# Kernel optimization log

Hardware: AMD Instinct MI355X
Metric: run time of the kernel (lower is better)

Reference implementation:

```python
import jax, jax.numpy as jnp
import numpy as np

B, T, P, D, H = 32, 64, 196, 768, 12
HD = D // H   # MHA head dim = 64
F = D // H    # GAT per-head out features = 64


def _grid_adj(num_patches):
    g = int(np.sqrt(num_patches))
    a = np.zeros((num_patches, num_patches), np.int32)
    for i in range(num_patches):
        a[i, i] = 1
        r, c = divmod(i, g)
        for dr in (-1, 0, 1):
            for dc in (-1, 0, 1):
                if dr == 0 and dc == 0:
                    continue
                nr, nc = r + dr, c + dc
                if 0 <= nr < g and 0 <= nc < g:
                    a[i, nr * g + nc] = 1
    return a


def setup_inputs():
    key = jax.random.key(0)
    ks = jax.random.split(key, 32)
    s = 0.02
    ta = jax.random.randint(ks[2], (B, T, T), 0, 2).astype(jnp.int32)
    ta = jnp.maximum(jnp.maximum(ta, ta.transpose(0, 2, 1)), jnp.eye(T, dtype=jnp.int32))
    return {
        'text_features': jax.random.normal(ks[0], (B, T, D), jnp.float32),
        'image_features': jax.random.normal(ks[1], (B, P, D), jnp.float32),
        'clip_text': jax.random.normal(ks[3], (B, 512), jnp.float32),
        'clip_image': jax.random.normal(ks[4], (B, 512), jnp.float32),
        'logit_scale': jnp.float32(4.6052),  # ln(100), CLIP default
        'wq': jax.random.normal(ks[5], (D, D), jnp.float32) * s,
        'bq': jnp.zeros((D,), jnp.float32),
        'wk': jax.random.normal(ks[6], (D, D), jnp.float32) * s,
        'bk': jnp.zeros((D,), jnp.float32),
        'wv': jax.random.normal(ks[7], (D, D), jnp.float32) * s,
        'bv': jnp.zeros((D,), jnp.float32),
        'wo': jax.random.normal(ks[8], (D, D), jnp.float32) * s,
        'bo': jnp.zeros((D,), jnp.float32),
        'Wt': jax.random.normal(ks[9], (D, H * F), jnp.float32) * s,
        'at': jax.random.normal(ks[10], (2 * F, 1), jnp.float32) * s,
        'Wi': jax.random.normal(ks[11], (D, H * F), jnp.float32) * s,
        'ai': jax.random.normal(ks[12], (2 * F, 1), jnp.float32) * s,
        'Wp': jax.random.normal(ks[13], (512, D), jnp.float32) * s,
        'bp': jnp.zeros((D,), jnp.float32),
        'f1w': jax.random.normal(ks[14], (3, 16), jnp.float32) * 0.3,
        'f1b': jnp.zeros((16,), jnp.float32),
        'f2w': jax.random.normal(ks[15], (16, 3), jnp.float32) * 0.3,
        'f2b': jnp.zeros((3,), jnp.float32),
        'c1w': jax.random.normal(ks[16], (D, D // 2), jnp.float32) * s,
        'c1b': jnp.zeros((D // 2,), jnp.float32),
        'c2w': jax.random.normal(ks[17], (D // 2, 2), jnp.float32) * s,
        'c2b': jnp.zeros((2,), jnp.float32),
        'text_adj': ta,
        'image_adj': jnp.asarray(_grid_adj(P)),
    }


def _gat(h, adj, W, a):
    # h: [N, D], adj: [N, N] (0/1), W: [D, H*F], a: [2F, 1]
    N = h.shape[0]
    Wh = (h @ W).reshape(N, H, F)
    # e_ij = leakyrelu(a^T [Wh_i ; Wh_j]) decomposed to avoid the N*N*2F concat tensor
    src = jnp.einsum('nhf,f->nh', Wh, a[:F, 0])   # [N, H]
    dst = jnp.einsum('nhf,f->nh', Wh, a[F:, 0])   # [N, H]
    e = jax.nn.leaky_relu(src[:, None, :] + dst[None, :, :], 0.2)  # [N, N, H]
    e = jnp.where(adj[:, :, None] > 0, e, jnp.float32(-9e15))
    att = jax.nn.softmax(e, axis=1)               # softmax over neighbors j
    hp = jnp.einsum('ijh,jhf->ihf', att, Wh)       # [N, H, F]
    return jax.nn.elu(hp.reshape(N, H * F))


def reference(text_features, image_features, clip_text, clip_image, logit_scale,
              wq, bq, wk, bk, wv, bv, wo, bo, Wt, at, Wi, ai, Wp, bp,
              f1w, f1b, f2w, f2b, c1w, c1b, c2w, c2b, text_adj, image_adj):
    # token-level cross attention (text queries, image keys/values)
    q = (text_features @ wq + bq).reshape(B, T, H, HD)
    k = (image_features @ wk + bk).reshape(B, P, H, HD)
    v = (image_features @ wv + bv).reshape(B, P, H, HD)
    scores = jnp.einsum('bthd,bphd->bhtp', q, k) / jnp.sqrt(jnp.float32(HD))
    upd = jnp.einsum('bhtp,bphd->bthd', jax.nn.softmax(scores, axis=-1), v)
    upd = upd.reshape(B, T, D) @ wo + bo           # [B, T, D]
    c = jnp.einsum('btd,bpd->btp', upd, image_features)
    s_token = jnp.mean(jnp.diagonal(c, axis1=-2, axis2=-1), axis=1)  # [B]
    f_token = upd.mean(axis=1)                     # [B, D]
    # per-sample GATs, batched via vmap
    tg = jax.vmap(lambda h, a_: _gat(h, a_, Wt, at))(text_features, text_adj)
    ig = jax.vmap(lambda h: _gat(h, image_adj, Wi, ai))(image_features)
    tgf = tg.mean(axis=1)
    igf = ig.mean(axis=1)

    def cos(x, y):
        nx = jnp.maximum(jnp.linalg.norm(x, axis=-1), 1e-8)
        ny = jnp.maximum(jnp.linalg.norm(y, axis=-1), 1e-8)
        return jnp.sum(x * y, axis=-1) / (nx * ny)

    s_phrase = cos(tgf, igf)
    s_global = jnp.exp(logit_scale) * cos(clip_text, clip_image)
    f_global = clip_text @ Wp + bp
    scores3 = jax.lax.stop_gradient(jnp.stack([s_token, s_phrase, s_global], axis=1))
    w = jax.nn.sigmoid(jax.nn.gelu(scores3 @ f1w + f1b, approximate=False) @ f2w + f2b)
    f_agg = w[:, 0:1] * f_token + w[:, 1:2] * tgf + w[:, 2:3] * f_global
    logits = jax.nn.relu(f_agg @ c1w + c1b) @ c2w + c2b  # dropout inactive (eval)
    return logits
```

## Files before the change

### kernel.cpp

```cpp
#include <hip/hip_runtime.h>
#include <hip/hip_bf16.h>
#include <math.h>

#define B 32
#define T 64
#define P 196
#define D 768
#define H 12

typedef __attribute__((ext_vector_type(8))) short short8;
typedef __attribute__((ext_vector_type(4))) float floatx4;

__device__ __forceinline__ float wave_sum(float v) {
#pragma unroll
  for (int o = 32; o > 0; o >>= 1) v += __shfl_xor(v, o);
  return v;
}
__device__ __forceinline__ unsigned short f2bf(float x) {
  unsigned u = __float_as_uint(x);
  u += 0x7FFFu + ((u >> 16) & 1u);
  return (unsigned short)(u >> 16);
}
__device__ __forceinline__ float bf2f(unsigned short x) {
  return __uint_as_float((unsigned)x << 16);
}
__device__ __forceinline__ float fexp(float x) { return __expf(x); }
__device__ __forceinline__ float frcp(float x) { return __builtin_amdgcn_rcpf(x); }
__device__ __forceinline__ void async_cp16(const unsigned short* g, unsigned short* l) {
  __builtin_amdgcn_global_load_lds(
      (const __attribute__((address_space(1))) unsigned int*)g,
      (__attribute__((address_space(3))) unsigned int*)l, 16, 0, 0);
}
__device__ __forceinline__ int xcd_remap(int orig, int nwg) {
  const int q = nwg >> 3, r = nwg & 7;
  const int x = orig & 7, o = orig >> 3;
  return (x < r ? x * (q + 1) : r * (q + 1) + (x - r) * q) + o;
}

struct WPack {
  const float* src[6];
  unsigned short* dst[6];
};
__global__ __launch_bounds__(256) void prep_kernel(
    WPack p,
    const float* __restrict__ text, unsigned short* __restrict__ text_bf, int n40,
    const float* __restrict__ img, unsigned short* __restrict__ img_bf, int n41,
    const float* __restrict__ bq, const float* __restrict__ bk,
    const float* __restrict__ bv,
    float* __restrict__ bt, float* __restrict__ bi, float* __restrict__ stok) {
  const int bid = blockIdx.x;
  if (bid < 3456) {
    __shared__ float tile[32][33];
    const int z = bid / 576, rem = bid % 576;
    const int bx = rem % 24, by = rem / 24;
    const float* W = p.src[z];
    unsigned short* Wt = p.dst[z];
    const int tx = threadIdx.x & 31, ty = threadIdx.x >> 5;
    const int n0 = bx * 32, k0 = by * 32;
#pragma unroll
    for (int r = 0; r < 4; ++r)
      tile[ty + 8 * r][tx] = W[(size_t)(k0 + ty + 8 * r) * D + n0 + tx];
    __syncthreads();
#pragma unroll
    for (int r = 0; r < 4; ++r)
      Wt[(size_t)(n0 + ty + 8 * r) * D + k0 + tx] = f2bf(tile[tx][ty + 8 * r]);
  } else if (bid < 9696) {
    int i = (bid - 3456) * 256 + threadIdx.x;
    const float* X;
    unsigned short* Y;
    int idx;
    if (i < n40) { X = text; Y = text_bf; idx = i; }
    else if (i < n40 + n41) { X = img; Y = img_bf; idx = i - n40; }
    else return;
    float4 vv = ((const float4*)X)[idx];
    ushort4 o;
    o.x = f2bf(vv.x); o.y = f2bf(vv.y); o.z = f2bf(vv.z); o.w = f2bf(vv.w);
    ((ushort4*)Y)[idx] = o;
  } else {
    int i = (bid - 9696) * 256 + threadIdx.x;
    if (i < 32) stok[i] = 0.f;
    if (i < 768) { bt[i] = bq[i]; bi[i] = bk[i]; }
    else if (i < 1536) { bt[i] = 0.f; bi[i] = bv[i - 768]; }
    else if (i < 2304) { bi[i] = 0.f; }
  }
}

struct GemmJob {
  const unsigned short* A;
  const unsigned short* Bt;
  const float* bias;
  void* C;
  int N, K, lda, ldb, colTiles;
};

template <bool BF16OUT>
__device__ __forceinline__ void gemm_body(const GemmJob& j, int bx, int by, int tid) {
  __shared__ unsigned short As[3][128][32];
  __shared__ unsigned short Bs[3][128][32];
  const int lane = tid & 63;
  const int w = tid >> 6;
  const int quad = lane >> 4;
  const int l15 = lane & 15;
  const int row0 = by * 128;
  const int col0 = bx * 128;
  const int m_off = (w & 1) * 64;
  const int n_off = (w >> 1) * 64;
  const int N = j.N, K = j.K;

  const int srow = 16 * w + (lane >> 2);
  const int scol = (((lane & 3) ^ ((lane >> 3) & 3))) * 8;
  const unsigned short* gA0 = j.A + (size_t)(row0 + srow) * j.lda + scol;
  const unsigned short* gA1 = j.A + (size_t)(row0 + srow + 64) * j.lda + scol;
  const unsigned short* gB0 = j.Bt + (size_t)(col0 + srow) * j.ldb + scol;
  const unsigned short* gB1 = j.Bt + (size_t)(col0 + srow + 64) * j.ldb + scol;

  const int rdc = (quad ^ ((l15 >> 1) & 3)) * 8;

  floatx4 acc[4][4] = {};
  short8 fA[4], fB_[4];
  short8 gA_[4], gB_[4];

#define STAGE(buf, kk)                                   \
  do {                                                   \
    async_cp16(gA0 + (kk), &As[buf][16 * w][0]);         \
    async_cp16(gA1 + (kk), &As[buf][64 + 16 * w][0]);    \
    async_cp16(gB0 + (kk), &Bs[buf][16 * w][0]);         \
    async_cp16(gB1 + (kk), &Bs[buf][64 + 16 * w][0]);    \
  } while (0)

  auto RD = [&](short8 (&AF)[4], short8 (&BF)[4], int buf) {
#pragma unroll
    for (int i = 0; i < 4; ++i)
      AF[i] = *(const short8*)&As[buf][m_off + 16 * i + l15][rdc];
#pragma unroll
    for (int j2 = 0; j2 < 4; ++j2)
      BF[j2] = *(const short8*)&Bs[buf][n_off + 16 * j2 + l15][rdc];
  };
  auto MM = [&](short8 (&AF)[4], short8 (&BF)[4]) {
#pragma unroll
    for (int i = 0; i < 4; ++i)
#pragma unroll
      for (int j2 = 0; j2 < 4; ++j2)
        acc[i][j2] = __builtin_amdgcn_mfma_f32_16x16x32_bf16(AF[i], BF[j2], acc[i][j2], 0, 0, 0);
  };
  auto PHASE = [&](short8 (&curA)[4], short8 (&curB)[4],
                   short8 (&nxtA)[4], short8 (&nxtB)[4],
                   int stageBuf, int readBuf, int kk) {
    if (kk + 64 < K) {
      STAGE(stageBuf, kk + 64);
      asm volatile("s_waitcnt vmcnt(4) lgkmcnt(0)" ::: "memory");
      __builtin_amdgcn_s_barrier();
      __builtin_amdgcn_sched_barrier(0);
      RD(nxtA, nxtB, readBuf);
    } else if (kk + 32 < K) {
      asm volatile("s_waitcnt vmcnt(0) lgkmcnt(0)" ::: "memory");
      __builtin_amdgcn_s_barrier();
      __builtin_amdgcn_sched_barrier(0);
      RD(nxtA, nxtB, readBuf);
    }
    MM(curA, curB);
  };

  STAGE(0, 0);
  STAGE(1, 32);
  asm volatile("s_waitcnt vmcnt(4)" ::: "memory");
  __builtin_amdgcn_s_barrier();
  __builtin_amdgcn_sched_barrier(0);
  RD(fA, fB_, 0);

  for (int k0 = 0; k0 < K; k0 += 192) {
    PHASE(fA, fB_, gA_, gB_, 2, 1, k0);
    PHASE(gA_, gB_, fA, fB_, 0, 2, k0 + 32);
    PHASE(fA, fB_, gA_, gB_, 1, 0, k0 + 64);
    PHASE(gA_, gB_, fA, fB_, 2, 1, k0 + 96);
    PHASE(fA, fB_, gA_, gB_, 0, 2, k0 + 128);
    PHASE(gA_, gB_, fA, fB_, 1, 0, k0 + 160);
  }
#undef STAGE

#pragma unroll
  for (int jj = 0; jj < 4; ++jj) {
    const int cg = col0 + n_off + 16 * jj + l15;
    const float bv = j.bias ? j.bias[cg] : 0.0f;
#pragma unroll
    for (int i = 0; i < 4; ++i) {
      const int rbase = row0 + m_off + 16 * i + quad * 4;
#pragma unroll
      for (int r = 0; r < 4; ++r) {
        const float val = acc[i][jj][r] + bv;
        const size_t idx = (size_t)(rbase + r) * N + cg;
        if (BF16OUT) ((unsigned short*)j.C)[idx] = f2bf(val);
        else ((float*)j.C)[idx] = val;
      }
    }
  }
}

__global__ __launch_bounds__(256) void gemm_mfma_dual_bf16(GemmJob j0, GemmJob j1,
                                                           int split, int total) {
  const bool first = ((int)blockIdx.x < split);
  const GemmJob& j = first ? j0 : j1;
  const int orig = first ? blockIdx.x : (blockIdx.x - split);
  const int bid = xcd_remap(orig, first ? split : total - split);
  const int bx = bid % j.colTiles;
  const int by = bid / j.colTiles;
  gemm_body<true>(j, bx, by, threadIdx.x);
}

__global__ __launch_bounds__(256) void gemm_mfma_dual_f32(GemmJob j0, GemmJob j1,
                                                          int split, int total) {
  const bool first = ((int)blockIdx.x < split);
  const GemmJob& j = first ? j0 : j1;
  const int orig = first ? blockIdx.x : (blockIdx.x - split);
  const int bid = xcd_remap(orig, first ? split : total - split);
  const int bx = bid % j.colTiles;
  const int by = bid / j.colTiles;
  gemm_body<false>(j, bx, by, threadIdx.x);
}


__device__ __forceinline__ void attn_body(
    char* smem, int h, int b,
    const unsigned short* __restrict__ qa, const unsigned short* __restrict__ kvw,
    unsigned short* __restrict__ attout) {
  const int tid = threadIdx.x, lane = tid & 63, w = tid >> 6;
  const int quad = lane >> 4, l15 = lane & 15;

  unsigned short (*Ks)[72] = (unsigned short(*)[72])smem;
  unsigned short (*Ps)[16][232] = (unsigned short(*)[16][232])smem;
  unsigned short (*VT)[232] = (unsigned short(*)[232])(smem + 29952);

  for (int i = tid; i < P * 8; i += 256) {
    const int p = i >> 3, dg = i & 7;
    const short8 k8 =
        *(const short8*)(kvw + (size_t)(b * P + p) * 2304 + h * 64 + dg * 8);
    *(short8*)&Ks[p][dg * 8] = k8;
  }
  {
    const int d = lane;
    const unsigned short* vbase = kvw + (size_t)b * P * 2304 + 768 + h * 64 + d;
    for (int pb = w; pb < 28; pb += 4) {
      short8 v;
#pragma unroll
      for (int z = 0; z < 8; ++z) {
        const int p = pb * 8 + z;
        v[z] = (p < P) ? (short)vbase[(size_t)p * 2304] : (short)0;
      }
      *(short8*)&VT[d][pb * 8] = v;
    }
  }
  __syncthreads();

  short8 aq[2];
#pragma unroll
  for (int ks = 0; ks < 2; ++ks)
    aq[ks] = *(const short8*)(qa + (size_t)(b * T + 16 * w + l15) * 1536 + h * 64 +
                              32 * ks + quad * 8);

  floatx4 sc[13];
#pragma unroll
  for (int tile = 0; tile < 13; ++tile) {
    int p = tile * 16 + l15;
    if (p > 195) p = 195;
    short8 bk0 = *(const short8*)&Ks[p][quad * 8];
    short8 bk1 = *(const short8*)&Ks[p][32 + quad * 8];
    floatx4 c = {};
    c = __builtin_amdgcn_mfma_f32_16x16x32_bf16(aq[0], bk0, c, 0, 0, 0);
    c = __builtin_amdgcn_mfma_f32_16x16x32_bf16(aq[1], bk1, c, 0, 0, 0);
    sc[tile] = c;
  }

  float mx[4] = {-3.4e38f, -3.4e38f, -3.4e38f, -3.4e38f};
#pragma unroll
  for (int tile = 0; tile < 13; ++tile)
#pragma unroll
    for (int r = 0; r < 4; ++r) {
      float s = sc[tile][r] * 0.125f;
      if (tile == 12 && l15 >= 4) s = -3.0e38f;
      sc[tile][r] = s;
      mx[r] = fmaxf(mx[r], s);
    }
#pragma unroll
  for (int off = 1; off < 16; off <<= 1)
#pragma unroll
    for (int r = 0; r < 4; ++r) mx[r] = fmaxf(mx[r], __shfl_xor(mx[r], off));

  float sm[4] = {};
#pragma unroll
  for (int tile = 0; tile < 13; ++tile)
#pragma unroll
    for (int r = 0; r < 4; ++r) {
      float e = fexp(sc[tile][r] - mx[r]);
      sc[tile][r] = e;
      sm[r] += e;
    }
#pragma unroll
  for (int off = 1; off < 16; off <<= 1)
#pragma unroll
    for (int r = 0; r < 4; ++r) sm[r] += __shfl_xor(sm[r], off);
  float inv[4];
#pragma unroll
  for (int r = 0; r < 4; ++r) inv[r] = frcp(sm[r]);

  __syncthreads();

#pragma unroll
  for (int tile = 0; tile < 13; ++tile)
#pragma unroll
    for (int r = 0; r < 4; ++r)
      Ps[w][quad * 4 + r][tile * 16 + l15] = f2bf(sc[tile][r]);
#pragma unroll
  for (int r = 0; r < 4; ++r)
    Ps[w][quad * 4 + r][208 + l15] = 0;

  floatx4 oc[4] = {};
#pragma unroll
  for (int ks = 0; ks < 7; ++ks) {
    short8 pa = *(const short8*)&Ps[w][l15][ks * 32 + quad * 8];
#pragma unroll
    for (int nt = 0; nt < 4; ++nt) {
      short8 bv = *(const short8*)&VT[nt * 16 + l15][ks * 32 + quad * 8];
      oc[nt] = __builtin_amdgcn_mfma_f32_16x16x32_bf16(pa, bv, oc[nt], 0, 0, 0);
    }
  }

#pragma unroll
  for (int nt = 0; nt < 4; ++nt)
#pragma unroll
    for (int r = 0; r < 4; ++r)
      attout[(size_t)(b * T + 16 * w + quad * 4 + r) * 768 + h * 64 + nt * 16 + l15] =
          f2bf(oc[nt][r] * inv[r]);
}

__device__ __forceinline__ void text_gat_body(
    char* smem, int h, int b,
    const unsigned short* __restrict__ Wh, int ldw, const int* __restrict__ adj,
    const float* __restrict__ at, float* __restrict__ tgf) {
  const int tid = threadIdx.x, lane = tid & 63, w = tid >> 6;
  const int quad = lane >> 4, l15 = lane & 15;

  unsigned short (*VT)[72] = (unsigned short(*)[72])smem;
  unsigned short (*Ps)[16][72] = (unsigned short(*)[16][72])(smem + 9216);
  float* srcs = (float*)(smem + 18432);
  float* dsts = (float*)(smem + 18688);
  float (*redc)[64] = (float(*)[64])(smem + 18944);
  float* asv = (float*)(smem + 19968);
  float* adv = (float*)(smem + 20224);

  if (tid < 64) { asv[tid] = at[tid]; adv[tid] = at[64 + tid]; }
  {
    const int f = lane;
    const unsigned short* wbase = Wh + (size_t)(b * T) * ldw + h * 64 + f;
    for (int nb = w; nb < 8; nb += 4) {
      short8 v;
#pragma unroll
      for (int z = 0; z < 8; ++z)
        v[z] = (short)wbase[(size_t)(nb * 8 + z) * ldw];
      *(short8*)&VT[f][nb * 8] = v;
    }
  }
  __syncthreads();

  if (tid < 64) {
    float s = 0.f, dd = 0.f;
#pragma unroll 8
    for (int f = 0; f < 64; ++f) {
      const float wv = bf2f(VT[f][tid]);
      s += wv * asv[f];
      dd += wv * adv[f];
    }
    srcs[tid] = s;
    dsts[tid] = dd;
  }
  __syncthreads();

  const int i = 16 * w + l15;
  const float si = srcs[i];
  const int* ar = adj + (size_t)b * T * T + i * 64;
  float sm = 0.f;
#pragma unroll 8
  for (int jj = 0; jj < 16; ++jj) {
    const int j = 4 * jj + quad;
    float e = si + dsts[j];
    e = (e >= 0.f) ? e : 0.2f * e;
    const float p = (ar[j] != 0) ? fexp(e) : 0.f;
    sm += p;
    Ps[w][l15][j] = f2bf(p);
  }
  sm += __shfl_xor(sm, 16);
  sm += __shfl_xor(sm, 32);
  const float inv = frcp(sm);

  floatx4 oc[4] = {};
#pragma unroll
  for (int ks = 0; ks < 2; ++ks) {
    const short8 pa = *(const short8*)&Ps[w][l15][ks * 32 + quad * 8];
#pragma unroll
    for (int nt = 0; nt < 4; ++nt) {
      const short8 bv = *(const short8*)&VT[nt * 16 + l15][ks * 32 + quad * 8];
      oc[nt] = __builtin_amdgcn_mfma_f32_16x16x32_bf16(pa, bv, oc[nt], 0, 0, 0);
    }
  }

  float accd[4] = {};
#pragma unroll
  for (int r = 0; r < 4; ++r) {
    const float invr = __shfl(inv, quad * 4 + r);
#pragma unroll
    for (int nt = 0; nt < 4; ++nt) {
      const float hp = oc[nt][r] * invr;
      accd[nt] += (hp > 0.f) ? hp : (fexp(hp) - 1.0f);
    }
  }
#pragma unroll
  for (int nt = 0; nt < 4; ++nt) {
    accd[nt] += __shfl_xor(accd[nt], 16);
    accd[nt] += __shfl_xor(accd[nt], 32);
  }
  if (quad == 0) {
#pragma unroll
    for (int nt = 0; nt < 4; ++nt) redc[w][nt * 16 + l15] = accd[nt];
  }
  __syncthreads();
  if (w == 0) {
    const float tot = redc[0][lane] + redc[1][lane] + redc[2][lane] + redc[3][lane];
    tgf[b * D + h * 64 + lane] = tot * (1.0f / T);
  }
}

__device__ __forceinline__ void image_gat_body(
    char* smem, int h, int b,
    const unsigned short* __restrict__ Wh, int ldw, const float* __restrict__ ai,
    const int* __restrict__ adj, float* __restrict__ igf) {
  const int tid = threadIdx.x, lane = tid & 63, w = tid >> 6;
  const int quad = lane >> 4, l15 = lane & 15;

  unsigned short (*VT)[232] = (unsigned short(*)[232])smem;
  unsigned short (*Ps)[232] = (unsigned short(*)[232])(smem + 29696);
  float* srcs = (float*)(smem + 37120);
  float* dsts = (float*)(smem + 37904);
  float* asv = (float*)(smem + 38688);
  float* adv = (float*)(smem + 38944);

  if (tid < 64) { asv[tid] = ai[tid]; adv[tid] = ai[64 + tid]; }
  {
    const int f = lane;
    const unsigned short* wbase = Wh + (size_t)(b * P) * ldw + h * 64 + f;
    for (int nb = w; nb < 28; nb += 4) {
      short8 v;
#pragma unroll
      for (int z = 0; z < 8; ++z) {
        const int p = nb * 8 + z;
        v[z] = (p < P) ? (short)wbase[(size_t)p * ldw] : (short)0;
      }
      *(short8*)&VT[f][nb * 8] = v;
    }
  }
  __syncthreads();

  if (tid < P) {
    float s = 0.f, dd = 0.f;
#pragma unroll 8
    for (int f = 0; f < 64; ++f) {
      const float wv = bf2f(VT[f][tid]);
      s += wv * asv[f];
      dd += wv * adv[f];
    }
    srcs[tid] = s;
    dsts[tid] = dd;
  }
  __syncthreads();

  const int rloc = tid >> 4;
  const int cslot = tid & 15;
  float accw = 0.f;

  for (int tile = 0; tile < 13; ++tile) {
    const int i = tile * 16 + rloc;
    const int ii = (i < P) ? i : (P - 1);
    const float si = srcs[ii];
    const int* ar = adj + ii * P;
    int msk[13];
#pragma unroll
    for (int k = 0; k < 13; ++k) {
      const int jc = k * 16 + cslot;
      msk[k] = (jc < P) ? ar[jc] : 0;
    }
    float pvv[13];
    float sm = 0.f;
#pragma unroll
    for (int k = 0; k < 13; ++k) {
      const int jc = k * 16 + cslot;
      float p = 0.f;
      if (jc < P && msk[k] != 0) {
        float e = si + dsts[jc];
        e = (e >= 0.f) ? e : 0.2f * e;
        p = fexp(e);
      }
      pvv[k] = p;
      sm += p;
    }
    sm += __shfl_xor(sm, 1);
    sm += __shfl_xor(sm, 2);
    sm += __shfl_xor(sm, 4);
    sm += __shfl_xor(sm, 8);
    const float inv = frcp(sm);
#pragma unroll
    for (int k = 0; k < 13; ++k)
      Ps[rloc][k * 16 + cslot] = f2bf(pvv[k] * inv);
    Ps[rloc][208 + cslot] = 0;
    __syncthreads();

    floatx4 oc = {};
#pragma unroll
    for (int ks = 0; ks < 7; ++ks) {
      const short8 pa = *(const short8*)&Ps[l15][ks * 32 + quad * 8];
      const short8 bvv = *(const short8*)&VT[w * 16 + l15][ks * 32 + quad * 8];
      oc = __builtin_amdgcn_mfma_f32_16x16x32_bf16(pa, bvv, oc, 0, 0, 0);
    }
#pragma unroll
    for (int r = 0; r < 4; ++r) {
      const int io = tile * 16 + quad * 4 + r;
      if (io < P) {
        const float hp = oc[r];
        accw += (hp > 0.f) ? hp : (fexp(hp) - 1.0f);
      }
    }
    __syncthreads();
  }

  accw += __shfl_xor(accw, 16);
  accw += __shfl_xor(accw, 32);
  if (quad == 0)
    igf[b * D + h * 64 + w * 16 + l15] = accw * (1.0f / P);
}

__device__ __forceinline__ void fglob_body(
    char* smem, int jt, int b,
    const float* __restrict__ clip_t, const float* __restrict__ Wp,
    const float* __restrict__ bp, float* __restrict__ fglob) {
  const int j = threadIdx.x & 63, kc = threadIdx.x >> 6;
  float s = 0.f;
  const float* ct = clip_t + b * 512;
#pragma unroll 4
  for (int k = kc * 128; k < kc * 128 + 128; ++k)
    s += ct[k] * Wp[(size_t)k * D + jt * 64 + j];
  float (*red)[64] = (float(*)[64])smem;
  red[kc][j] = s;
  __syncthreads();
  if (kc == 0)
    fglob[b * D + jt * 64 + j] = red[0][j] + red[1][j] + red[2][j] + red[3][j] + bp[jt * 64 + j];
}

__global__ __launch_bounds__(256) void mid_kernel(
    const unsigned short* __restrict__ qa_bf, const unsigned short* __restrict__ kvw_bf,
    unsigned short* __restrict__ att_bf,
    const int* __restrict__ text_adj, const float* __restrict__ at,
    float* __restrict__ tgf,
    const unsigned short* __restrict__ whi, int ldw_i,
    const float* __restrict__ ai, const int* __restrict__ image_adj,
    float* __restrict__ igf,
    const float* __restrict__ clip_t, const float* __restrict__ Wp,
    const float* __restrict__ bp, float* __restrict__ fglob) {
  __shared__ __align__(16) char smem[59648];
  const int h = blockIdx.x, b = blockIdx.y, op = blockIdx.z;
  if (op == 0)
    attn_body(smem, h, b, qa_bf, kvw_bf, att_bf);
  else if (op == 1)
    text_gat_body(smem, h, b, qa_bf + 768, 1536, text_adj, at, tgf);
  else if (op == 2)
    image_gat_body(smem, h, b, whi, ldw_i, ai, image_adj, igf);
  else
    fglob_body(smem, h, b, clip_t, Wp, bp, fglob);
}

__global__ __launch_bounds__(256) void token_kernel(
    const float* __restrict__ upd0, const float* __restrict__ upd1,
    const float* __restrict__ img,
    float* __restrict__ f_token, float* __restrict__ s_token) {
  const int jt = blockIdx.x, b = blockIdx.y;
  const int l = threadIdx.x & 63, tg = threadIdx.x >> 6;
  const int d = jt * 64 + l;
  float fs = 0.f, ss = 0.f;
#pragma unroll 4
  for (int tt = 0; tt < 16; ++tt) {
    const int t = tg * 16 + tt;
    const size_t idx = (size_t)(b * T + t) * D + d;
    const float u = upd0[idx] + upd1[idx];
    fs += u;
    ss += u * img[(size_t)(b * P + t) * D + d];
  }
  __shared__ float red[4][64];
  __shared__ float sred[4];
  red[tg][l] = fs;
  const float sw = wave_sum(ss);
  if (l == 0) sred[tg] = sw;
  __syncthreads();
  if (tg == 0) {
    f_token[(size_t)b * D + d] =
        (red[0][l] + red[1][l] + red[2][l] + red[3][l]) * (1.0f / T);
    if (threadIdx.x == 0)
      atomicAdd(&s_token[b], (sred[0] + sred[1] + sred[2] + sred[3]) * (1.0f / T));
  }
}

__global__ __launch_bounds__(256) void xc1_kernel(
    const float* __restrict__ ftok, const float* __restrict__ tgf,
    const float* __restrict__ fglob, const float* __restrict__ c1w,
    float* __restrict__ Xc) {
  const int jt = blockIdx.x;
  const int r = blockIdx.y;
  const int b = r & 31, which = r >> 5;
  const float* src = (which == 0 ? ftok : which == 1 ? tgf : fglob) + (size_t)b * D;
  const int j = threadIdx.x & 63, kc = threadIdx.x >> 6;
  const int col = jt * 64 + j;
  float s = 0.f;
#pragma unroll 4
  for (int k = kc * 192; k < kc * 192 + 192; ++k)
    s += src[k] * c1w[(size_t)k * 384 + col];
  __shared__ float red[4][64];
  red[kc][j] = s;
  __syncthreads();
  if (kc == 0)
    Xc[(size_t)r * 384 + col] = red[0][j] + red[1][j] + red[2][j] + red[3][j];
}

__device__ __forceinline__ float block_sum(float v, float* red4) {
  v = wave_sum(v);
  __syncthreads();
  if ((threadIdx.x & 63) == 0) red4[threadIdx.x >> 6] = v;
  __syncthreads();
  return red4[0] + red4[1] + red4[2] + red4[3];
}

__global__ __launch_bounds__(256) void final_kernel(
    const float* __restrict__ tgf, const float* __restrict__ igf,
    const float* __restrict__ clip_t, const float* __restrict__ clip_i,
    const float* __restrict__ logit_scale, const float* __restrict__ s_token,
    const float* __restrict__ Xc,
    const float* __restrict__ f1w, const float* __restrict__ f1b,
    const float* __restrict__ f2w, const float* __restrict__ f2b,
    const float* __restrict__ c1b,
    const float* __restrict__ c2w, const float* __restrict__ c2b,
    float* __restrict__ out) {
  const int b = blockIdx.x, tid = threadIdx.x;
  __shared__ float red[4];
  __shared__ float sres[4];
  __shared__ float hid[384];

  float d0 = 0.f, d1 = 0.f, d2 = 0.f;
  for (int i = tid; i < D; i += 256) {
    float x = tgf[b * D + i], y = igf[b * D + i];
    d0 += x * y; d1 += x * x; d2 += y * y;
  }
  float dot_ti = block_sum(d0, red);
  float n_t = sqrtf(block_sum(d1, red));
  float n_i = sqrtf(block_sum(d2, red));
  float s_phrase = dot_ti / (fmaxf(n_t, 1e-8f) * fmaxf(n_i, 1e-8f));

  float c0 = 0.f, c1 = 0.f, c2 = 0.f;
  for (int i = tid; i < 512; i += 256) {
    float x = clip_t[b * 512 + i], y = clip_i[b * 512 + i];
    c0 += x * y; c1 += x * x; c2 += y * y;
  }
  float dc = block_sum(c0, red);
  float nt2 = sqrtf(block_sum(c1, red));
  float ni2 = sqrtf(block_sum(c2, red));
  float s_global = expf(logit_scale[0]) * dc / (fmaxf(nt2, 1e-8f) * fmaxf(ni2, 1e-8f));

  if (tid == 0) {
    float s3[3] = { s_token[b], s_phrase, s_global };
    float h1[16];
    for (int j = 0; j < 16; ++j) {
      float a = f1b[j];
      for (int i2 = 0; i2 < 3; ++i2) a += s3[i2] * f1w[i2 * 16 + j];
      h1[j] = 0.5f * a * (1.0f + erff(a * 0.70710678118654752f));
    }
    for (int j = 0; j < 3; ++j) {
      float a = f2b[j];
      for (int i2 = 0; i2 < 16; ++i2) a += h1[i2] * f2w[i2 * 3 + j];
      sres[j] = 1.0f / (1.0f + expf(-a));
    }
  }
  __syncthreads();
  const float w0 = sres[0], w1 = sres[1], w2 = sres[2];

  for (int j = tid; j < 384; j += 256) {
    const float a = w0 * Xc[(size_t)b * 384 + j] +
                    w1 * Xc[(size_t)(32 + b) * 384 + j] +
                    w2 * Xc[(size_t)(64 + b) * 384 + j] + c1b[j];
    hid[j] = fmaxf(a, 0.0f);
  }
  __syncthreads();

  float p0 = 0.f, p1 = 0.f;
  for (int k2 = tid; k2 < 384; k2 += 256) {
    p0 += hid[k2] * c2w[k2 * 2 + 0];
    p1 += hid[k2] * c2w[k2 * 2 + 1];
  }
  p0 = block_sum(p0, red);
  p1 = block_sum(p1, red);
  if (tid == 0) {
    out[b * 2 + 0] = p0 + c2b[0];
    out[b * 2 + 1] = p1 + c2b[1];
  }
}

extern "C" void kernel_launch(void* const* d_in, const int* in_sizes, int n_in,
                              void* d_out, int out_size, void* d_ws, size_t ws_size,
                              hipStream_t stream) {
  const float* text   = (const float*)d_in[0];
  const float* img    = (const float*)d_in[1];
  const float* clip_t = (const float*)d_in[2];
  const float* clip_i = (const float*)d_in[3];
  const float* lscale = (const float*)d_in[4];
  const float* wq = (const float*)d_in[5];
  const float* bq = (const float*)d_in[6];
  const float* wk = (const float*)d_in[7];
  const float* bk = (const float*)d_in[8];
  const float* wv = (const float*)d_in[9];
  const float* bv = (const float*)d_in[10];
  const float* wo = (const float*)d_in[11];
  const float* bo = (const float*)d_in[12];
  const float* Wt = (const float*)d_in[13];
  const float* at = (const float*)d_in[14];
  const float* Wi = (const float*)d_in[15];
  const float* ai = (const float*)d_in[16];
  const float* Wp = (const float*)d_in[17];
  const float* bp = (const float*)d_in[18];
  const float* f1w = (const float*)d_in[19];
  const float* f1b = (const float*)d_in[20];
  const float* f2w = (const float*)d_in[21];
  const float* f2b = (const float*)d_in[22];
  const float* c1w = (const float*)d_in[23];
  const float* c1b = (const float*)d_in[24];
  const float* c2w = (const float*)d_in[25];
  const float* c2b = (const float*)d_in[26];
  const int* text_adj  = (const int*)d_in[27];
  const int* image_adj = (const int*)d_in[28];
  float* out = (float*)d_out;

  const size_t nTD = (size_t)B * T * D;
  const size_t nPD = (size_t)B * P * D;
  const size_t nWW = (size_t)D * D;

  float* fbuf = (float*)d_ws;
  size_t o = 0;
  float* upd0    = fbuf + o; o += nTD;
  float* upd1    = fbuf + o; o += nTD;
  float* ftok    = fbuf + o; o += (size_t)B * D;
  float* stok    = fbuf + o; o += 32;
  float* tgf     = fbuf + o; o += (size_t)B * D;
  float* igf     = fbuf + o; o += (size_t)B * D;
  float* fglob   = fbuf + o; o += (size_t)B * D;
  float* bcat_t  = fbuf + o; o += 1536;
  float* bcat_i3 = fbuf + o; o += 2304;
  float* Xc      = fbuf + o; o += (size_t)96 * 384;
  unsigned short* sbuf = (unsigned short*)(fbuf + o);
  size_t so = 0;
  unsigned short* kvw_bf    = sbuf + so; so += 3 * nPD;
  unsigned short* qa_bf     = sbuf + so; so += 2 * nTD;
  unsigned short* text_bf   = sbuf + so; so += nTD;
  unsigned short* img_bf    = sbuf + so; so += nPD;
  unsigned short* att_bf    = sbuf + so; so += nTD;
  unsigned short* wcat_txt  = sbuf + so; so += 2 * nWW;
  unsigned short* wcat_img3 = sbuf + so; so += 3 * nWW;
  unsigned short* wo_t      = sbuf + so; so += nWW;

  WPack wp;
  wp.src[0] = wq; wp.dst[0] = wcat_txt;
  wp.src[1] = Wt; wp.dst[1] = wcat_txt + nWW;
  wp.src[2] = wk; wp.dst[2] = wcat_img3;
  wp.src[3] = wv; wp.dst[3] = wcat_img3 + nWW;
  wp.src[4] = Wi; wp.dst[4] = wcat_img3 + 2 * nWW;
  wp.src[5] = wo; wp.dst[5] = wo_t;
  {
    const int n40 = (int)(nTD / 4), n41 = (int)(nPD / 4);
    prep_kernel<<<9708, 256, 0, stream>>>(wp, text, text_bf, n40, img, img_bf, n41,
                                          bq, bk, bv, bcat_t, bcat_i3, stok);
  }

  const int MT = B * T;
  const int MP = B * P;

  GemmJob jimg;
  jimg.A = img_bf; jimg.Bt = wcat_img3; jimg.bias = bcat_i3; jimg.C = kvw_bf;
  jimg.N = 2304; jimg.K = D; jimg.lda = D; jimg.ldb = D; jimg.colTiles = 2304 / 128;
  GemmJob jtxt;
  jtxt.A = text_bf; jtxt.Bt = wcat_txt; jtxt.bias = bcat_t; jtxt.C = qa_bf;
  jtxt.N = 1536; jtxt.K = D; jtxt.lda = D; jtxt.ldb = D; jtxt.colTiles = 1536 / 128;
  const int splitBlocks = (2304 / 128) * (MP / 128);
  const int totalBlocks = splitBlocks + (1536 / 128) * (MT / 128);
  gemm_mfma_dual_bf16<<<totalBlocks, 256, 0, stream>>>(jimg, jtxt, splitBlocks, totalBlocks);

  const unsigned short* whi_bf = kvw_bf + 1536;
  mid_kernel<<<dim3(H, B, 4), 256, 0, stream>>>(
      qa_bf, kvw_bf, att_bf,
      text_adj, at, tgf,
      whi_bf, 2304, ai, image_adj, igf,
      clip_t, Wp, bp, fglob);

  GemmJob jwo0;
  jwo0.A = att_bf; jwo0.Bt = wo_t; jwo0.bias = bo; jwo0.C = upd0;
  jwo0.N = D; jwo0.K = 384; jwo0.lda = D; jwo0.ldb = D; jwo0.colTiles = D / 128;
  GemmJob jwo1;
  jwo1.A = att_bf + 384; jwo1.Bt = wo_t + 384; jwo1.bias = nullptr; jwo1.C = upd1;
  jwo1.N = D; jwo1.K = 384; jwo1.lda = D; jwo1.ldb = D; jwo1.colTiles = D / 128;
  const int woHalf = (D / 128) * (MT / 128);
  gemm_mfma_dual_f32<<<2 * woHalf, 256, 0, stream>>>(jwo0, jwo1, woHalf, 2 * woHalf);

  token_kernel<<<dim3(12, B), 256, 0, stream>>>(upd0, upd1, img, ftok, stok);
  xc1_kernel<<<dim3(6, 96), 256, 0, stream>>>(ftok, tgf, fglob, c1w, Xc);
  final_kernel<<<B, 256, 0, stream>>>(tgf, igf, clip_t, clip_i, lscale, stok, Xc,
                                      f1w, f1b, f2w, f2b, c1b, c2w, c2b, out);
}
```

Measured before the change: 260.9 us.

## Split wo GEMM four-way along K, move fglob to prep kernel

The output-projection GEMM is now split into four K=192 slices instead of two K=384 slices, so more blocks are in flight on the small M=2048 problem, and the token kernel sums four partial buffers. The clip-text projection (fglob) moves out of mid_kernel into extra blocks of prep_kernel, taking it off the attention/GAT stage. The Q-fragment load in attention is hoisted ahead of the K/V shared-memory staging, and the xc1 and fglob dot loops use four independent accumulators. In exchange, two extra fp32 partial buffers must be written and then read back, which adds memory traffic.

```diff
diff --git a/kernel.cpp b/kernel.cpp
--- a/kernel.cpp
+++ b/kernel.cpp
@@ -47,7 +47,9 @@
     const float* __restrict__ img, unsigned short* __restrict__ img_bf, int n41,
     const float* __restrict__ bq, const float* __restrict__ bk,
     const float* __restrict__ bv,
-    float* __restrict__ bt, float* __restrict__ bi, float* __restrict__ stok) {
+    float* __restrict__ bt, float* __restrict__ bi, float* __restrict__ stok,
+    const float* __restrict__ clip_t, const float* __restrict__ Wp,
+    const float* __restrict__ bp, float* __restrict__ fglob) {
   const int bid = blockIdx.x;
   if (bid < 3456) {
     __shared__ float tile[32][33];
@@ -76,12 +78,32 @@
     ushort4 o;
     o.x = f2bf(vv.x); o.y = f2bf(vv.y); o.z = f2bf(vv.z); o.w = f2bf(vv.w);
     ((ushort4*)Y)[idx] = o;
-  } else {
+  } else if (bid < 9708) {
     int i = (bid - 9696) * 256 + threadIdx.x;
     if (i < 32) stok[i] = 0.f;
     if (i < 768) { bt[i] = bq[i]; bi[i] = bk[i]; }
     else if (i < 1536) { bt[i] = 0.f; bi[i] = bv[i - 768]; }
     else if (i < 2304) { bi[i] = 0.f; }
+  } else {
+    __shared__ float red[4][64];
+    const int bid2 = bid - 9708;
+    const int jt = bid2 % 12, b = bid2 / 12;
+    const int j = threadIdx.x & 63, kc = threadIdx.x >> 6;
+    const float* ct = clip_t + b * 512 + kc * 128;
+    const float* wp = Wp + (size_t)(kc * 128) * D + jt * 64 + j;
+    float s0 = 0.f, s1 = 0.f, s2 = 0.f, s3 = 0.f;
+#pragma unroll
+    for (int k = 0; k < 128; k += 4) {
+      s0 += ct[k]     * wp[(size_t)k * D];
+      s1 += ct[k + 1] * wp[(size_t)(k + 1) * D];
+      s2 += ct[k + 2] * wp[(size_t)(k + 2) * D];
+      s3 += ct[k + 3] * wp[(size_t)(k + 3) * D];
+    }
+    red[kc][j] = (s0 + s1) + (s2 + s3);
+    __syncthreads();
+    if (kc == 0)
+      fglob[b * D + jt * 64 + j] =
+          red[0][j] + red[1][j] + red[2][j] + red[3][j] + bp[jt * 64 + j];
   }
 }
 
@@ -207,12 +229,13 @@
   gemm_body<true>(j, bx, by, threadIdx.x);
 }
 
-__global__ __launch_bounds__(256) void gemm_mfma_dual_f32(GemmJob j0, GemmJob j1,
-                                                          int split, int total) {
-  const bool first = ((int)blockIdx.x < split);
-  const GemmJob& j = first ? j0 : j1;
-  const int orig = first ? blockIdx.x : (blockIdx.x - split);
-  const int bid = xcd_remap(orig, first ? split : total - split);
+__global__ __launch_bounds__(256) void gemm_mfma_quad_f32(GemmJob j0, GemmJob j1,
+                                                          GemmJob j2, GemmJob j3,
+                                                          int per) {
+  const int which = (int)blockIdx.x / per;
+  const GemmJob& j = (which == 0) ? j0 : (which == 1) ? j1 : (which == 2) ? j2 : j3;
+  const int orig = (int)blockIdx.x - which * per;
+  const int bid = xcd_remap(orig, per);
   const int bx = bid % j.colTiles;
   const int by = bid / j.colTiles;
   gemm_body<false>(j, bx, by, threadIdx.x);
@@ -230,6 +253,12 @@
   unsigned short (*Ps)[16][232] = (unsigned short(*)[16][232])smem;
   unsigned short (*VT)[232] = (unsigned short(*)[232])(smem + 29952);
 
+  short8 aq[2];
+#pragma unroll
+  for (int ks = 0; ks < 2; ++ks)
+    aq[ks] = *(const short8*)(qa + (size_t)(b * T + 16 * w + l15) * 1536 + h * 64 +
+                              32 * ks + quad * 8);
+
   for (int i = tid; i < P * 8; i += 256) {
     const int p = i >> 3, dg = i & 7;
     const short8 k8 =
@@ -250,12 +279,6 @@
     }
   }
   __syncthreads();
-
-  short8 aq[2];
-#pragma unroll
-  for (int ks = 0; ks < 2; ++ks)
-    aq[ks] = *(const short8*)(qa + (size_t)(b * T + 16 * w + l15) * 1536 + h * 64 +
-                              32 * ks + quad * 8);
 
   floatx4 sc[13];
 #pragma unroll
@@ -535,23 +558,6 @@
     igf[b * D + h * 64 + w * 16 + l15] = accw * (1.0f / P);
 }
 
-__device__ __forceinline__ void fglob_body(
-    char* smem, int jt, int b,
-    const float* __restrict__ clip_t, const float* __restrict__ Wp,
-    const float* __restrict__ bp, float* __restrict__ fglob) {
-  const int j = threadIdx.x & 63, kc = threadIdx.x >> 6;
-  float s = 0.f;
-  const float* ct = clip_t + b * 512;
-#pragma unroll 4
-  for (int k = kc * 128; k < kc * 128 + 128; ++k)
-    s += ct[k] * Wp[(size_t)k * D + jt * 64 + j];
-  float (*red)[64] = (float(*)[64])smem;
-  red[kc][j] = s;
-  __syncthreads();
-  if (kc == 0)
-    fglob[b * D + jt * 64 + j] = red[0][j] + red[1][j] + red[2][j] + red[3][j] + bp[jt * 64 + j];
-}
-
 __global__ __launch_bounds__(256) void mid_kernel(
     const unsigned short* __restrict__ qa_bf, const unsigned short* __restrict__ kvw_bf,
     unsigned short* __restrict__ att_bf,
@@ -559,23 +565,20 @@
     float* __restrict__ tgf,
     const unsigned short* __restrict__ whi, int ldw_i,
     const float* __restrict__ ai, const int* __restrict__ image_adj,
-    float* __restrict__ igf,
-    const float* __restrict__ clip_t, const float* __restrict__ Wp,
-    const float* __restrict__ bp, float* __restrict__ fglob) {
+    float* __restrict__ igf) {
   __shared__ __align__(16) char smem[59648];
   const int h = blockIdx.x, b = blockIdx.y, op = blockIdx.z;
   if (op == 0)
     attn_body(smem, h, b, qa_bf, kvw_bf, att_bf);
   else if (op == 1)
     text_gat_body(smem, h, b, qa_bf + 768, 1536, text_adj, at, tgf);
-  else if (op == 2)
+  else
     image_gat_body(smem, h, b, whi, ldw_i, ai, image_adj, igf);
-  else
-    fglob_body(smem, h, b, clip_t, Wp, bp, fglob);
 }
 
 __global__ __launch_bounds__(256) void token_kernel(
     const float* __restrict__ upd0, const float* __restrict__ upd1,
+    const float* __restrict__ upd2, const float* __restrict__ upd3,
     const float* __restrict__ img,
     float* __restrict__ f_token, float* __restrict__ s_token) {
   const int jt = blockIdx.x, b = blockIdx.y;
@@ -586,7 +589,7 @@
   for (int tt = 0; tt < 16; ++tt) {
     const int t = tg * 16 + tt;
     const size_t idx = (size_t)(b * T + t) * D + d;
-    const float u = upd0[idx] + upd1[idx];
+    const float u = (upd0[idx] + upd1[idx]) + (upd2[idx] + upd3[idx]);
     fs += u;
     ss += u * img[(size_t)(b * P + t) * D + d];
   }
@@ -614,12 +617,18 @@
   const float* src = (which == 0 ? ftok : which == 1 ? tgf : fglob) + (size_t)b * D;
   const int j = threadIdx.x & 63, kc = threadIdx.x >> 6;
   const int col = jt * 64 + j;
-  float s = 0.f;
-#pragma unroll 4
-  for (int k = kc * 192; k < kc * 192 + 192; ++k)
-    s += src[k] * c1w[(size_t)k * 384 + col];
+  const float* cw = c1w + (size_t)(kc * 192) * 384 + col;
+  const float* sk = src + kc * 192;
+  float s0 = 0.f, s1 = 0.f, s2 = 0.f, s3 = 0.f;
+#pragma unroll 12
+  for (int k = 0; k < 192; k += 4) {
+    s0 += sk[k]     * cw[(size_t)k * 384];
+    s1 += sk[k + 1] * cw[(size_t)(k + 1) * 384];
+    s2 += sk[k + 2] * cw[(size_t)(k + 2) * 384];
+    s3 += sk[k + 3] * cw[(size_t)(k + 3) * 384];
+  }
   __shared__ float red[4][64];
-  red[kc][j] = s;
+  red[kc][j] = (s0 + s1) + (s2 + s3);
   __syncthreads();
   if (kc == 0)
     Xc[(size_t)r * 384 + col] = red[0][j] + red[1][j] + red[2][j] + red[3][j];
@@ -748,6 +757,8 @@
   size_t o = 0;
   float* upd0    = fbuf + o; o += nTD;
   float* upd1    = fbuf + o; o += nTD;
+  float* upd2    = fbuf + o; o += nTD;
+  float* upd3    = fbuf + o; o += nTD;
   float* ftok    = fbuf + o; o += (size_t)B * D;
   float* stok    = fbuf + o; o += 32;
   float* tgf     = fbuf + o; o += (size_t)B * D;
@@ -776,8 +787,9 @@
   wp.src[5] = wo; wp.dst[5] = wo_t;
   {
     const int n40 = (int)(nTD / 4), n41 = (int)(nPD / 4);
-    prep_kernel<<<9708, 256, 0, stream>>>(wp, text, text_bf, n40, img, img_bf, n41,
-                                          bq, bk, bv, bcat_t, bcat_i3, stok);
+    prep_kernel<<<10092, 256, 0, stream>>>(wp, text, text_bf, n40, img, img_bf, n41,
+                                           bq, bk, bv, bcat_t, bcat_i3, stok,
+                                           clip_t, Wp, bp, fglob);
   }
 
   const int MT = B * T;
@@ -794,22 +806,23 @@
   gemm_mfma_dual_bf16<<<totalBlocks, 256, 0, stream>>>(jimg, jtxt, splitBlocks, totalBlocks);
 
   const unsigned short* whi_bf = kvw_bf + 1536;
-  mid_kernel<<<dim3(H, B, 4), 256, 0, stream>>>(
+  mid_kernel<<<dim3(H, B, 3), 256, 0, stream>>>(
       qa_bf, kvw_bf, att_bf,
       text_adj, at, tgf,
-      whi_bf, 2304, ai, image_adj, igf,
-      clip_t, Wp, bp, fglob);
-
-  GemmJob jwo0;
-  jwo0.A = att_bf; jwo0.Bt = wo_t; jwo0.bias = bo; jwo0.C = upd0;
-  jwo0.N = D; jwo0.K = 384; jwo0.lda = D; jwo0.ldb = D; jwo0.colTiles = D / 128;
-  GemmJob jwo1;
-  jwo1.A = att_bf + 384; jwo1.Bt = wo_t + 384; jwo1.bias = nullptr; jwo1.C = upd1;
-  jwo1.N = D; jwo1.K = 384; jwo1.lda = D; jwo1.ldb = D; jwo1.colTiles = D / 128;
-  const int woHalf = (D / 128) * (MT / 128);
-  gemm_mfma_dual_f32<<<2 * woHalf, 256, 0, stream>>>(jwo0, jwo1, woHalf, 2 * woHalf);
-
-  token_kernel<<<dim3(12, B), 256, 0, stream>>>(upd0, upd1, img, ftok, stok);
+      whi_bf, 2304, ai, image_adj, igf);
+
+  GemmJob jw[4];
+  for (int k = 0; k < 4; ++k) {
+    jw[k].A = att_bf + k * 192;
+    jw[k].Bt = wo_t + k * 192;
+    jw[k].bias = (k == 0) ? bo : nullptr;
+    jw[k].C = (k == 0) ? upd0 : (k == 1) ? upd1 : (k == 2) ? upd2 : upd3;
+    jw[k].N = D; jw[k].K = 192; jw[k].lda = D; jw[k].ldb = D; jw[k].colTiles = D / 128;
+  }
+  const int woPer = (D / 128) * (MT / 128);
+  gemm_mfma_quad_f32<<<4 * woPer, 256, 0, stream>>>(jw[0], jw[1], jw[2], jw[3], woPer);
+
+  token_kernel<<<dim3(12, B), 256, 0, stream>>>(upd0, upd1, upd2, upd3, img, ftok, stok);
   xc1_kernel<<<dim3(6, 96), 256, 0, stream>>>(ftok, tgf, fglob, c1w, Xc);
   final_kernel<<<B, 256, 0, stream>>>(tgf, igf, clip_t, clip_i, lscale, stok, Xc,
                                       f1w, f1b, f2w, f2b, c1b, c2w, c2b, out);
```

Result: slower. 270.1 us (+3.5%).

## Split attention out of mid kernel and co-schedule Wo GEMM with GAT branches

Applied to the files above, without the earlier changes.

Attention now runs in its own kernel. The output-projection GEMM is merged into one launch with the text GAT, image GAT and CLIP projection blocks, so the independent GAT work overlaps with the Wo GEMM instead of waiting behind the attention stage. The Q fragment load in attention is also hoisted ahead of the K/V shared-memory staging so its global latency can overlap. The combined kernel sizes shared memory at 48KB for every branch, which assumes the GAT bodies fit in that space, and heterogeneous block types share one launch.

```diff
diff --git a/kernel.cpp b/kernel.cpp
--- a/kernel.cpp
+++ b/kernel.cpp
@@ -94,9 +94,10 @@
 };
 
 template <bool BF16OUT>
-__device__ __forceinline__ void gemm_body(const GemmJob& j, int bx, int by, int tid) {
-  __shared__ unsigned short As[3][128][32];
-  __shared__ unsigned short Bs[3][128][32];
+__device__ __forceinline__ void gemm_body(const GemmJob& j, int bx, int by, int tid,
+                                          char* smem) {
+  unsigned short (*As)[128][32] = (unsigned short(*)[128][32])smem;
+  unsigned short (*Bs)[128][32] = (unsigned short(*)[128][32])(smem + 24576);
   const int lane = tid & 63;
   const int w = tid >> 6;
   const int quad = lane >> 4;
@@ -198,24 +199,14 @@
 
 __global__ __launch_bounds__(256) void gemm_mfma_dual_bf16(GemmJob j0, GemmJob j1,
                                                            int split, int total) {
+  __shared__ __align__(16) char gsmem[49152];
   const bool first = ((int)blockIdx.x < split);
   const GemmJob& j = first ? j0 : j1;
   const int orig = first ? blockIdx.x : (blockIdx.x - split);
   const int bid = xcd_remap(orig, first ? split : total - split);
   const int bx = bid % j.colTiles;
   const int by = bid / j.colTiles;
-  gemm_body<true>(j, bx, by, threadIdx.x);
-}
-
-__global__ __launch_bounds__(256) void gemm_mfma_dual_f32(GemmJob j0, GemmJob j1,
-                                                          int split, int total) {
-  const bool first = ((int)blockIdx.x < split);
-  const GemmJob& j = first ? j0 : j1;
-  const int orig = first ? blockIdx.x : (blockIdx.x - split);
-  const int bid = xcd_remap(orig, first ? split : total - split);
-  const int bx = bid % j.colTiles;
-  const int by = bid / j.colTiles;
-  gemm_body<false>(j, bx, by, threadIdx.x);
+  gemm_body<true>(j, bx, by, threadIdx.x, gsmem);
 }
 
 
@@ -230,6 +221,12 @@
   unsigned short (*Ps)[16][232] = (unsigned short(*)[16][232])smem;
   unsigned short (*VT)[232] = (unsigned short(*)[232])(smem + 29952);
 
+  short8 aq[2];
+#pragma unroll
+  for (int ks = 0; ks < 2; ++ks)
+    aq[ks] = *(const short8*)(qa + (size_t)(b * T + 16 * w + l15) * 1536 + h * 64 +
+                              32 * ks + quad * 8);
+
   for (int i = tid; i < P * 8; i += 256) {
     const int p = i >> 3, dg = i & 7;
     const short8 k8 =
@@ -250,12 +247,6 @@
     }
   }
   __syncthreads();
-
-  short8 aq[2];
-#pragma unroll
-  for (int ks = 0; ks < 2; ++ks)
-    aq[ks] = *(const short8*)(qa + (size_t)(b * T + 16 * w + l15) * 1536 + h * 64 +
-                              32 * ks + quad * 8);
 
   floatx4 sc[13];
 #pragma unroll
@@ -330,6 +321,13 @@
     for (int r = 0; r < 4; ++r)
       attout[(size_t)(b * T + 16 * w + quad * 4 + r) * 768 + h * 64 + nt * 16 + l15] =
           f2bf(oc[nt][r] * inv[r]);
+}
+
+__global__ __launch_bounds__(256) void attn_kernel(
+    const unsigned short* __restrict__ qa_bf, const unsigned short* __restrict__ kvw_bf,
+    unsigned short* __restrict__ att_bf) {
+  __shared__ __align__(16) char smem[59648];
+  attn_body(smem, blockIdx.x, blockIdx.y, qa_bf, kvw_bf, att_bf);
 }
 
 __device__ __forceinline__ void text_gat_body(
@@ -552,9 +550,9 @@
     fglob[b * D + jt * 64 + j] = red[0][j] + red[1][j] + red[2][j] + red[3][j] + bp[jt * 64 + j];
 }
 
-__global__ __launch_bounds__(256) void mid_kernel(
-    const unsigned short* __restrict__ qa_bf, const unsigned short* __restrict__ kvw_bf,
-    unsigned short* __restrict__ att_bf,
+__global__ __launch_bounds__(256) void combo_kernel(
+    GemmJob jwo0, GemmJob jwo1,
+    const unsigned short* __restrict__ qa_bf,
     const int* __restrict__ text_adj, const float* __restrict__ at,
     float* __restrict__ tgf,
     const unsigned short* __restrict__ whi, int ldw_i,
@@ -562,16 +560,24 @@
     float* __restrict__ igf,
     const float* __restrict__ clip_t, const float* __restrict__ Wp,
     const float* __restrict__ bp, float* __restrict__ fglob) {
-  __shared__ __align__(16) char smem[59648];
-  const int h = blockIdx.x, b = blockIdx.y, op = blockIdx.z;
-  if (op == 0)
-    attn_body(smem, h, b, qa_bf, kvw_bf, att_bf);
-  else if (op == 1)
-    text_gat_body(smem, h, b, qa_bf + 768, 1536, text_adj, at, tgf);
-  else if (op == 2)
-    image_gat_body(smem, h, b, whi, ldw_i, ai, image_adj, igf);
-  else
-    fglob_body(smem, h, b, clip_t, Wp, bp, fglob);
+  __shared__ __align__(16) char smem[49152];
+  const int bid = blockIdx.x;
+  if (bid < 192) {
+    const bool first = bid < 96;
+    const GemmJob& j = first ? jwo0 : jwo1;
+    const int orig = first ? bid : bid - 96;
+    const int b2 = xcd_remap(orig, 96);
+    gemm_body<false>(j, b2 % j.colTiles, b2 / j.colTiles, threadIdx.x, smem);
+  } else if (bid < 576) {
+    const int idx = bid - 192;
+    text_gat_body(smem, idx % 12, idx / 12, qa_bf + 768, 1536, text_adj, at, tgf);
+  } else if (bid < 960) {
+    const int idx = bid - 576;
+    image_gat_body(smem, idx % 12, idx / 12, whi, ldw_i, ai, image_adj, igf);
+  } else {
+    const int idx = bid - 960;
+    fglob_body(smem, idx % 12, idx / 12, clip_t, Wp, bp, fglob);
+  }
 }
 
 __global__ __launch_bounds__(256) void token_kernel(
@@ -793,12 +799,7 @@
   const int totalBlocks = splitBlocks + (1536 / 128) * (MT / 128);
   gemm_mfma_dual_bf16<<<totalBlocks, 256, 0, stream>>>(jimg, jtxt, splitBlocks, totalBlocks);
 
-  const unsigned short* whi_bf = kvw_bf + 1536;
-  mid_kernel<<<dim3(H, B, 4), 256, 0, stream>>>(
-      qa_bf, kvw_bf, att_bf,
-      text_adj, at, tgf,
-      whi_bf, 2304, ai, image_adj, igf,
-      clip_t, Wp, bp, fglob);
+  attn_kernel<<<dim3(H, B), 256, 0, stream>>>(qa_bf, kvw_bf, att_bf);
 
   GemmJob jwo0;
   jwo0.A = att_bf; jwo0.Bt = wo_t; jwo0.bias = bo; jwo0.C = upd0;
@@ -806,8 +807,12 @@
   GemmJob jwo1;
   jwo1.A = att_bf + 384; jwo1.Bt = wo_t + 384; jwo1.bias = nullptr; jwo1.C = upd1;
   jwo1.N = D; jwo1.K = 384; jwo1.lda = D; jwo1.ldb = D; jwo1.colTiles = D / 128;
-  const int woHalf = (D / 128) * (MT / 128);
-  gemm_mfma_dual_f32<<<2 * woHalf, 256, 0, stream>>>(jwo0, jwo1, woHalf, 2 * woHalf);
+  const unsigned short* whi_bf = kvw_bf + 1536;
+  combo_kernel<<<1344, 256, 0, stream>>>(
+      jwo0, jwo1,
+      qa_bf, text_adj, at, tgf,
+      whi_bf, 2304, ai, image_adj, igf,
+      clip_t, Wp, bp, fglob);
 
   token_kernel<<<dim3(12, B), 256, 0, stream>>>(upd0, upd1, img, ftok, stok);
   xc1_kernel<<<dim3(6, 96), 256, 0, stream>>>(ftok, tgf, fglob, c1w, Xc);
```

New measurement: 263.0 us. About the same (+0.8%).
